# Kernel optimization log

Measured on AMD Instinct MI355X. Metric: run time of the kernel, lower is better.

## Reference

```python
import jax, jax.numpy as jnp
import numpy as np

# batched graph: B graphs, each with N_PER_G nodes, fixed in-degree DEG
N_NODES = 51200
N_PER_G = 100
B = 512
DEG = 16
E = N_NODES * DEG
D_IN = 100   # input node feature dim
H1 = 100     # gc1 out
D_G = 20     # gc2 out / graph embedding dim
D_K = 32
P2D = 200    # dim_self_feat
P3D = 100    # dim_3d_feat
D_OUT = 1
LN_EPS = 1e-5


def setup_inputs() -> dict:
    key = jax.random.key(0)
    ks = jax.random.split(key, 24)
    feat = jax.random.normal(ks[0], (N_NODES, D_IN), jnp.float32)
    # every node has exactly DEG in-edges; sources drawn within the same graph
    edge_dst = jnp.repeat(jnp.arange(N_NODES, dtype=jnp.int32), DEG)
    off = jax.random.randint(ks[1], (E,), 0, N_PER_G, jnp.int32)
    edge_src = (edge_dst // N_PER_G) * N_PER_G + off
    self_feat = jax.random.normal(ks[2], (B, P2D), jnp.float32)
    x3d = jax.random.normal(ks[3], (B, P3D), jnp.float32)

    def lin(k, o, i):
        return jax.random.normal(k, (o, i), jnp.float32) / np.sqrt(i).astype(np.float32)

    params = dict(
        W1=lin(ks[4], H1, D_IN), b1=jnp.zeros((H1,), jnp.float32),
        W2=lin(ks[5], D_G, H1), b2=jnp.zeros((D_G,), jnp.float32),
        Wq2=lin(ks[6], D_K, D_G), Wk2=lin(ks[7], D_K, P2D),
        Wv2=lin(ks[8], D_K, P2D), Wo2=lin(ks[9], D_G, D_K),
        g2=jnp.ones((D_G,), jnp.float32), be2=jnp.zeros((D_G,), jnp.float32),
        Wq3=lin(ks[10], D_K, D_G), Wk3=lin(ks[11], D_K, P3D),
        Wv3=lin(ks[12], D_K, P3D), Wo3=lin(ks[13], D_G, D_K),
        g3=jnp.ones((D_G,), jnp.float32), be3=jnp.zeros((D_G,), jnp.float32),
        Wf1=lin(ks[14], 10, D_G), bf1=jnp.zeros((10,), jnp.float32),
        Wf2=lin(ks[15], D_OUT, 10), bf2=jnp.zeros((D_OUT,), jnp.float32),
    )
    return dict(feat=feat, edge_src=edge_src, edge_dst=edge_dst,
                self_feat=self_feat, x3d=x3d, **params)


def _gcn(h, src, dst, W, b):
    # copy_u -> mailbox mean (every node has exactly DEG in-edges) -> Linear
    msg = h[src]                                              # [E, d] gather
    acc = jax.ops.segment_sum(msg, dst, num_segments=N_NODES) / DEG
    return acc @ W.T + b


def _cross_attn(hg, x, Wq, Wk, Wv, Wo, gamma, beta):
    # K,V are single tokens -> softmax over length-1 axis is identically 1
    # so Z = V @ Wo^T exactly (Q/Wq does not affect the output values).
    Z = (x @ Wv.T) @ Wo.T                                     # [B, d_g]
    y = hg + Z
    mu = jnp.mean(y, axis=-1, keepdims=True)
    var = jnp.mean((y - mu) ** 2, axis=-1, keepdims=True)
    hg_attn = (y - mu) / jnp.sqrt(var + LN_EPS) * gamma + beta
    A = jnp.ones((hg.shape[0], 1), y.dtype)                   # softmax of (B,1,1)
    return hg_attn, A


def reference(feat, edge_src, edge_dst, self_feat, x3d,
              W1, b1, W2, b2,
              Wq2, Wk2, Wv2, Wo2, g2, be2,
              Wq3, Wk3, Wv3, Wo3, g3, be3,
              Wf1, bf1, Wf2, bf2):
    h = jax.nn.relu(_gcn(feat, edge_src, edge_dst, W1, b1))   # [N, 100]
    h = jax.nn.relu(_gcn(h, edge_src, edge_dst, W2, b2))      # [N, 20]
    hg = h.reshape(B, N_PER_G, D_G).mean(axis=1)              # dgl.mean_nodes
    hg1, _ = _cross_attn(hg, self_feat, Wq2, Wk2, Wv2, Wo2, g2, be2)
    hg2, _ = _cross_attn(hg1, x3d, Wq3, Wk3, Wv3, Wo3, g3, be3)
    out = jax.nn.relu(hg2 @ Wf1.T + bf1)
    out = out @ Wf2.T + bf2                                   # [B, 1]
    return out
```

## Files before the change

kernel.cpp:

```cpp
#include <hip/hip_runtime.h>
#include <hip/hip_bf16.h>

#define LN_EPS 1e-5f

typedef __attribute__((ext_vector_type(8))) short bf16x8;
typedef __attribute__((ext_vector_type(4))) float f32x4;

#define S 136
#define OFF_F  0
#define OFF_A  13600
#define OFF_S  28832
#define OFF_T2 33184
#define FLT    37536
#define ARENA_U 39360

#define FSF  0
#define FX3  200
#define FB1  300
#define FB2  400
#define FG2  420
#define FBE2 440
#define FG3  460
#define FBE3 480
#define FWF1 500
#define FBF1 700
#define FWF2 712
#define FBF2 724
#define FV2  728
#define FV3  760
#define FZ2  792
#define FZ3  812
#define FHGP 832

__device__ __forceinline__ unsigned short bf16rne(float x) {
    union { float f; unsigned u; } v; v.f = x;
    unsigned r = (v.u + 0x7FFFu + ((v.u >> 16) & 1u)) >> 16;
    return (unsigned short)r;
}

__device__ __forceinline__ unsigned pk2(float a, float b) {
    __hip_bfloat162 h = __float22bfloat162_rn(float2{a, b});
    unsigned r; __builtin_memcpy(&r, &h, 4); return r;
}

__device__ __forceinline__ void st4bf(unsigned short* p, const f32x4 v) {
    *(uint2*)p = make_uint2(pk2(v[0], v[1]), pk2(v[2], v[3]));
}

__device__ __forceinline__ bf16x8 pk8(const float4 a, const float4 b) {
    union { bf16x8 v; uint4 u; } r;
    r.u = make_uint4(pk2(a.x, a.y), pk2(a.z, a.w), pk2(b.x, b.y), pk2(b.z, b.w));
    return r.v;
}

template<int NT>
__device__ __forceinline__ void gemm_row(const unsigned short* __restrict__ ar,
    int Abase, int Bbase, int mrow, int lm, int lq, f32x4 (&acc)[NT])
{
    #pragma unroll
    for (int ks = 0; ks < 4; ++ks) {
        const int k = ks * 32 + lq * 8;
        bf16x8 a = *(const bf16x8*)&ar[Abase + (mrow * 16 + lm) * S + k];
        #pragma unroll
        for (int n = 0; n < NT; ++n) {
            bf16x8 b = *(const bf16x8*)&ar[Bbase + (n * 16 + lm) * S + k];
            acc[n] = __builtin_amdgcn_mfma_f32_16x16x32_bf16(a, b, acc[n], 0, 0, 0);
        }
    }
}

__global__ __launch_bounds__(512, 4) void fused_net_v6(
    const float* __restrict__ feat, const int* __restrict__ edge_src,
    const float* __restrict__ self_feat, const float* __restrict__ x3d,
    const float* __restrict__ W1, const float* __restrict__ b1,
    const float* __restrict__ W2, const float* __restrict__ b2,
    const float* __restrict__ Wv2, const float* __restrict__ Wo2,
    const float* __restrict__ g2, const float* __restrict__ be2,
    const float* __restrict__ Wv3, const float* __restrict__ Wo3,
    const float* __restrict__ g3, const float* __restrict__ be3,
    const float* __restrict__ Wf1, const float* __restrict__ bf1,
    const float* __restrict__ Wf2, const float* __restrict__ bf2,
    float* __restrict__ out)
{
    __shared__ __align__(16) unsigned short ar[ARENA_U];
    float* fl = (float*)&ar[FLT];

    const int g    = blockIdx.x;
    const int tid  = threadIdx.x;
    const int w    = tid >> 6;
    const int lane = tid & 63;
    const int lm   = lane & 15;
    const int lq   = lane >> 4;

    int arow = -1;
    if (w == 7) arow = lane;
    else if (w == 6 && lane < 36) arow = 64 + lane;
    int er[16];
    bf16x8 afrag[4];

    {
        if (w < 7) {
            int am = w * 16 + lm; if (am > 99) am = 99;
            const float* frow = feat + g * 10000 + am * 100;
            #pragma unroll
            for (int ks = 0; ks < 3; ++ks) {
                const int k = ks * 32 + lq * 8;
                const float4 a = *(const float4*)&frow[k];
                const float4 b = *(const float4*)&frow[k + 4];
                afrag[ks] = pk8(a, b);
            }
            if (lq == 0) {
                const float4 a = *(const float4*)&frow[96];
                afrag[3] = pk8(a, make_float4(0.f, 0.f, 0.f, 0.f));
            } else {
                union { bf16x8 v; uint4 u; } z; z.u = make_uint4(0u,0u,0u,0u);
                afrag[3] = z.v;
            }
        }

        if (tid < 50) *(float4*)&fl[FSF + tid * 4] = *(const float4*)&self_feat[g * 200 + tid * 4];
        else if (tid < 75)  *(float4*)&fl[FX3 + (tid - 50) * 4] = *(const float4*)&x3d[g * 100 + (tid - 50) * 4];
        else if (tid < 100) *(float4*)&fl[FB1 + (tid - 75) * 4] = *(const float4*)&b1[(tid - 75) * 4];
        else if (tid < 105) *(float4*)&fl[FB2 + (tid - 100) * 4] = *(const float4*)&b2[(tid - 100) * 4];
        else if (tid < 110) *(float4*)&fl[FG2 + (tid - 105) * 4] = *(const float4*)&g2[(tid - 105) * 4];
        else if (tid < 115) *(float4*)&fl[FBE2 + (tid - 110) * 4] = *(const float4*)&be2[(tid - 110) * 4];
        else if (tid < 120) *(float4*)&fl[FG3 + (tid - 115) * 4] = *(const float4*)&g3[(tid - 115) * 4];
        else if (tid < 125) *(float4*)&fl[FBE3 + (tid - 120) * 4] = *(const float4*)&be3[(tid - 120) * 4];
        else if (tid < 175) *(float4*)&fl[FWF1 + (tid - 125) * 4] = *(const float4*)&Wf1[(tid - 125) * 4];
        else if (tid < 185) { const int j = tid - 175; fl[FBF1 + j] = bf1[j]; fl[FWF2 + j] = Wf2[j]; }
        else if (tid == 185) fl[FBF2] = bf2[0];
        if (tid >= 256 && tid < 336) fl[FHGP + (tid - 256)] = 0.f;

        if (arow >= 0) {
            const int* ep = edge_src + g * 1600 + arow * 16;
            int4 e;
            e = *(const int4*)&ep[0];  er[0]=e.x;  er[1]=e.y;  er[2]=e.z;  er[3]=e.w;
            e = *(const int4*)&ep[4];  er[4]=e.x;  er[5]=e.y;  er[6]=e.z;  er[7]=e.w;
            e = *(const int4*)&ep[8];  er[8]=e.x;  er[9]=e.y;  er[10]=e.z; er[11]=e.w;
            e = *(const int4*)&ep[12]; er[12]=e.x; er[13]=e.y; er[14]=e.z; er[15]=e.w;
            const int base = g * 100;
            #pragma unroll
            for (int i = 0; i < 16; ++i) er[i] -= base;
        }

        for (int i = tid; i < 2500; i += 512) {
            const int n = i / 25, k4 = (i % 25) * 4;
            const float4 v = *(const float4*)&W1[n * 100 + k4];
            *(uint2*)&ar[OFF_A + n * S + k4] = make_uint2(pk2(v.x, v.y), pk2(v.z, v.w));
        }
        for (int i = tid; i < 700; i += 512) {
            const int n = i / 7, j = (i % 7) * 4;
            *(uint2*)&ar[OFF_A + n * S + 100 + j] = make_uint2(0u, 0u);
        }
        for (int i = tid; i < 700; i += 512) {
            const int n = i / 7, j = (i % 7) * 4;
            *(uint2*)&ar[OFF_F + n * S + 100 + j] = make_uint2(0u, 0u);
        }
        for (int i = tid; i < 500; i += 512) {
            const int n = i / 25, k4 = (i % 25) * 4;
            const float4 v = *(const float4*)&W2[n * 100 + k4];
            *(uint2*)&ar[OFF_S + n * S + k4] = make_uint2(pk2(v.x, v.y), pk2(v.z, v.w));
        }
        for (int i = tid; i < 140; i += 512) {
            const int n = i / 7, j = (i % 7) * 4;
            *(uint2*)&ar[OFF_S + n * S + 100 + j] = make_uint2(0u, 0u);
        }
        for (int i = tid; i < 140; i += 512) {
            const int n = i / 7, j = (i % 7) * 4;
            *(uint2*)&ar[OFF_T2 + n * S + 100 + j] = make_uint2(0u, 0u);
        }
    }
    __syncthreads();

    f32x4 acc[7];
    {
        const f32x4 z = {0.f, 0.f, 0.f, 0.f};
        #pragma unroll
        for (int n = 0; n < 7; ++n) acc[n] = z;
    }
    if (w < 7) {
        #pragma unroll
        for (int ks = 0; ks < 4; ++ks) {
            const int k = ks * 32 + lq * 8;
            #pragma unroll
            for (int n = 0; n < 7; ++n) {
                bf16x8 b = *(const bf16x8*)&ar[OFF_A + (n * 16 + lm) * S + k];
                acc[n] = __builtin_amdgcn_mfma_f32_16x16x32_bf16(afrag[ks], b, acc[n], 0, 0, 0);
            }
        }
    } else {
        const int j = lane >> 1, h = lane & 1;
        {
            const float* wr = Wv2 + j * 200 + h * 100;
            float s = 0.f;
            for (int c = 0; c < 25; ++c) {
                const float4 a = *(const float4*)&wr[c * 4];
                const float4 x = *(const float4*)&fl[FSF + h * 100 + c * 4];
                s += a.x * x.x + a.y * x.y + a.z * x.z + a.w * x.w;
            }
            s += __shfl_xor(s, 1);
            if (h == 0) fl[FV2 + j] = s;
        }
        {
            const float* wr = Wv3 + j * 100;
            const int c0 = h ? 13 : 0, c1 = h ? 25 : 13;
            float s = 0.f;
            for (int c = c0; c < c1; ++c) {
                const float4 a = *(const float4*)&wr[c * 4];
                const float4 x = *(const float4*)&fl[FX3 + c * 4];
                s += a.x * x.x + a.y * x.y + a.z * x.z + a.w * x.w;
            }
            s += __shfl_xor(s, 1);
            if (h == 0) fl[FV3 + j] = s;
        }
    }
    __syncthreads();

    if (w < 7) {
        const int m0 = w * 16 + lq * 4;
        #pragma unroll
        for (int n = 0; n < 7; ++n) {
            const int cc = n * 16 + lm;
            if (cc < 100 && m0 <= 96) st4bf(&ar[OFF_F + cc * S + m0], acc[n]);
        }
    }
    if (arow >= 0) {
        const uint4 z4i = make_uint4(0u, 0u, 0u, 0u);
        const int st = arow & 7;
        #pragma unroll
        for (int pp = 0; pp < 17; ++pp) {
            int p = pp + st; if (p >= 17) p -= 17;
            *(uint4*)&ar[OFF_A + arow * S + p * 8] = z4i;
        }
        #pragma unroll
        for (int i = 0; i < 16; ++i) {
            int cnt = 0;
            #pragma unroll
            for (int j = 0; j < 16; ++j) cnt += (er[j] == er[i]);
            ar[OFF_A + arow * S + er[i]] = bf16rne((float)cnt * 0.0625f);
        }
    }
    __syncthreads();

    {
        const f32x4 z = {0.f, 0.f, 0.f, 0.f};
        #pragma unroll
        for (int n = 0; n < 7; ++n) acc[n] = z;
    }
    if (w < 7) {
        gemm_row<7>(ar, OFF_F, OFF_A, w, lm, lq, acc);
    } else {
        if (lane < 20) {
            const float* wr = Wo2 + lane * 32;
            float s = 0.f;
            #pragma unroll
            for (int c = 0; c < 8; ++c) {
                const float4 a = *(const float4*)&wr[c * 4];
                s += a.x * fl[FV2 + c * 4] + a.y * fl[FV2 + c * 4 + 1]
                   + a.z * fl[FV2 + c * 4 + 2] + a.w * fl[FV2 + c * 4 + 3];
            }
            fl[FZ2 + lane] = s;
        } else if (lane < 40) {
            const int j = lane - 20;
            const float* wr = Wo3 + j * 32;
            float s = 0.f;
            #pragma unroll
            for (int c = 0; c < 8; ++c) {
                const float4 a = *(const float4*)&wr[c * 4];
                s += a.x * fl[FV3 + c * 4] + a.y * fl[FV3 + c * 4 + 1]
                   + a.z * fl[FV3 + c * 4 + 2] + a.w * fl[FV3 + c * 4 + 3];
            }
            fl[FZ3 + j] = s;
        }
    }
    __syncthreads();

    if (w < 7) {
        const int m0 = w * 16 + lq * 4;
        if (m0 <= 96) {
            const float4 bb = *(const float4*)&fl[FB1 + m0];
            #pragma unroll
            for (int n = 0; n < 7; ++n) {
                const int cc = n * 16 + lm;
                if (cc < 100) {
                    f32x4 v = acc[n];
                    v[0] = fmaxf(v[0] + bb.x, 0.f); v[1] = fmaxf(v[1] + bb.y, 0.f);
                    v[2] = fmaxf(v[2] + bb.z, 0.f); v[3] = fmaxf(v[3] + bb.w, 0.f);
                    st4bf(&ar[OFF_F + cc * S + m0], v);
                }
            }
        }
    }
    __syncthreads();

    const int mt  = w & 1;
    const int ntA = w >> 1;
    const bool hasB = (w < 6);
    const int ntB = 4 + (w >> 1);
    {
        const f32x4 z = {0.f, 0.f, 0.f, 0.f};
        f32x4 cA = z, cB = z;
        #pragma unroll
        for (int ks = 0; ks < 4; ++ks) {
            const int k = ks * 32 + lq * 8;
            bf16x8 a = *(const bf16x8*)&ar[OFF_S + (mt * 16 + lm) * S + k];
            bf16x8 bA = *(const bf16x8*)&ar[OFF_F + (ntA * 16 + lm) * S + k];
            cA = __builtin_amdgcn_mfma_f32_16x16x32_bf16(a, bA, cA, 0, 0, 0);
            if (hasB) {
                bf16x8 bB = *(const bf16x8*)&ar[OFF_F + (ntB * 16 + lm) * S + k];
                cB = __builtin_amdgcn_mfma_f32_16x16x32_bf16(a, bB, cB, 0, 0, 0);
            }
        }
        const int ccA = ntA * 16 + lm;
        if (ccA < 100) {
            #pragma unroll
            for (int r = 0; r < 4; ++r) {
                const int f2 = mt * 16 + lq * 4 + r;
                if (f2 < 20) ar[OFF_T2 + f2 * S + ccA] = bf16rne(cA[r]);
            }
        }
        if (hasB) {
            const int ccB = ntB * 16 + lm;
            if (ccB < 100) {
                #pragma unroll
                for (int r = 0; r < 4; ++r) {
                    const int f2 = mt * 16 + lq * 4 + r;
                    if (f2 < 20) ar[OFF_T2 + f2 * S + ccB] = bf16rne(cB[r]);
                }
            }
        }
    }
    __syncthreads();

    {
        const f32x4 z = {0.f, 0.f, 0.f, 0.f};
        f32x4 cA = z, cB = z;
        #pragma unroll
        for (int ks = 0; ks < 4; ++ks) {
            const int k = ks * 32 + lq * 8;
            bf16x8 a = *(const bf16x8*)&ar[OFF_T2 + (mt * 16 + lm) * S + k];
            bf16x8 bA = *(const bf16x8*)&ar[OFF_A + (ntA * 16 + lm) * S + k];
            cA = __builtin_amdgcn_mfma_f32_16x16x32_bf16(a, bA, cA, 0, 0, 0);
            if (hasB) {
                bf16x8 bB = *(const bf16x8*)&ar[OFF_A + (ntB * 16 + lm) * S + k];
                cB = __builtin_amdgcn_mfma_f32_16x16x32_bf16(a, bB, cB, 0, 0, 0);
            }
        }
        const int ccA = ntA * 16 + lm;
        const int ccB = ntB * 16 + lm;
        #pragma unroll
        for (int r = 0; r < 4; ++r) {
            const int f2 = mt * 16 + lq * 4 + r;
            const bool fv = (f2 < 20);
            const float bias = fv ? fl[FB2 + (fv ? f2 : 0)] : 0.f;
            float val = (fv && ccA < 100) ? fmaxf(cA[r] + bias, 0.f) : 0.f;
            if (hasB && fv && ccB < 100) val += fmaxf(cB[r] + bias, 0.f);
            val += __shfl_xor(val, 1);
            val += __shfl_xor(val, 2);
            val += __shfl_xor(val, 4);
            val += __shfl_xor(val, 8);
            if (lm == 0 && fv) fl[FHGP + (w >> 1) * 20 + f2] = val;
        }
    }
    __syncthreads();

    if (tid < 64) {
        const int j = tid;
        float y = 0.f;
        if (j < 20) {
            y = fl[FHGP + j] + fl[FHGP + 20 + j] + fl[FHGP + 40 + j] + fl[FHGP + 60 + j];
            y = y * 0.01f + fl[FZ2 + j];
        }
        float s = y;
        s += __shfl_xor(s, 1); s += __shfl_xor(s, 2); s += __shfl_xor(s, 4);
        s += __shfl_xor(s, 8); s += __shfl_xor(s, 16);
        const float mu = s * 0.05f;
        float d = (j < 20) ? (y - mu) : 0.f;
        float v = d * d;
        v += __shfl_xor(v, 1); v += __shfl_xor(v, 2); v += __shfl_xor(v, 4);
        v += __shfl_xor(v, 8); v += __shfl_xor(v, 16);
        const float inv1 = 1.f / sqrtf(v * 0.05f + LN_EPS);
        float y2 = 0.f;
        if (j < 20) y2 = d * inv1 * fl[FG2 + j] + fl[FBE2 + j] + fl[FZ3 + j];
        float s2 = y2;
        s2 += __shfl_xor(s2, 1); s2 += __shfl_xor(s2, 2); s2 += __shfl_xor(s2, 4);
        s2 += __shfl_xor(s2, 8); s2 += __shfl_xor(s2, 16);
        const float mu2 = s2 * 0.05f;
        float d2 = (j < 20) ? (y2 - mu2) : 0.f;
        float v2 = d2 * d2;
        v2 += __shfl_xor(v2, 1); v2 += __shfl_xor(v2, 2); v2 += __shfl_xor(v2, 4);
        v2 += __shfl_xor(v2, 8); v2 += __shfl_xor(v2, 16);
        const float inv2 = 1.f / sqrtf(v2 * 0.05f + LN_EPS);
        float y3 = 0.f;
        if (j < 20) y3 = d2 * inv2 * fl[FG3 + j] + fl[FBE3 + j];

        float acc7 = 0.f;
        {
            const int js = (j < 10) ? j : 0;
            #pragma unroll
            for (int k = 0; k < 20; ++k) {
                const float yk = __shfl(y3, k);
                acc7 += fl[FWF1 + js * 20 + k] * yk;
            }
            const float bias = fl[FBF1 + js];
            const float w2v  = fl[FWF2 + js];
            acc7 = (j < 10) ? fmaxf(acc7 + bias, 0.f) * w2v : 0.f;
        }
        acc7 += __shfl_xor(acc7, 1); acc7 += __shfl_xor(acc7, 2);
        acc7 += __shfl_xor(acc7, 4); acc7 += __shfl_xor(acc7, 8);
        if (j == 0) out[g] = acc7 + fl[FBF2];
    }
}

extern "C" void kernel_launch(void* const* d_in, const int* in_sizes, int n_in,
                              void* d_out, int out_size, void* d_ws, size_t ws_size,
                              hipStream_t stream) {
    const float* feat      = (const float*)d_in[0];
    const int*   edge_src  = (const int*)  d_in[1];
    const float* self_feat = (const float*)d_in[3];
    const float* x3d       = (const float*)d_in[4];
    const float* W1  = (const float*)d_in[5];
    const float* b1  = (const float*)d_in[6];
    const float* W2  = (const float*)d_in[7];
    const float* b2  = (const float*)d_in[8];
    const float* Wv2 = (const float*)d_in[11];
    const float* Wo2 = (const float*)d_in[12];
    const float* g2  = (const float*)d_in[13];
    const float* be2 = (const float*)d_in[14];
    const float* Wv3 = (const float*)d_in[17];
    const float* Wo3 = (const float*)d_in[18];
    const float* g3  = (const float*)d_in[19];
    const float* be3 = (const float*)d_in[20];
    const float* Wf1 = (const float*)d_in[21];
    const float* bf1 = (const float*)d_in[22];
    const float* Wf2 = (const float*)d_in[23];
    const float* bf2 = (const float*)d_in[24];

    fused_net_v6<<<512, 512, 0, stream>>>(feat, edge_src, self_feat, x3d,
                                          W1, b1, W2, b2,
                                          Wv2, Wo2, g2, be2,
                                          Wv3, Wo3, g3, be3,
                                          Wf1, bf1, Wf2, bf2,
                                          (float*)d_out);
}
```

Baseline: 130.2 us.

## Load W1 fragments directly from global and merge prologue phases to drop barriers

The first GEMM now builds its B fragments for W1 directly from global memory into registers instead of staging W1 as bf16 in shared memory. That removes a barrier and lets the X@W1 product and the adjacency-matrix build run in the same phase. The cross-attention V projections read self_feat and x3d straight from global, and the adjacency rows are built by wave 7 with per-lane register edge lists. Two __syncthreads are removed, at the cost of redundant global W1 loads per wave, which the cache should serve.

```diff
diff --git a/kernel.cpp b/kernel.cpp
--- a/kernel.cpp
+++ b/kernel.cpp
@@ -14,8 +14,6 @@
 #define FLT    37536
 #define ARENA_U 39360
 
-#define FSF  0
-#define FX3  200
 #define FB1  300
 #define FB2  400
 #define FG2  420
@@ -69,7 +67,7 @@
     }
 }
 
-__global__ __launch_bounds__(512, 4) void fused_net_v6(
+__global__ __launch_bounds__(512, 4) void fused_net_v7(
     const float* __restrict__ feat, const int* __restrict__ edge_src,
     const float* __restrict__ self_feat, const float* __restrict__ x3d,
     const float* __restrict__ W1, const float* __restrict__ b1,
@@ -92,110 +90,121 @@
     const int lm   = lane & 15;
     const int lq   = lane >> 4;
 
-    int arow = -1;
-    if (w == 7) arow = lane;
-    else if (w == 6 && lane < 36) arow = 64 + lane;
-    int er[16];
-    bf16x8 afrag[4];
-
-    {
-        if (w < 7) {
+    if (tid < 25)       *(float4*)&fl[FB1 + tid * 4]          = *(const float4*)&b1[tid * 4];
+    else if (tid < 30)  *(float4*)&fl[FB2 + (tid - 25) * 4]   = *(const float4*)&b2[(tid - 25) * 4];
+    else if (tid < 35)  *(float4*)&fl[FG2 + (tid - 30) * 4]   = *(const float4*)&g2[(tid - 30) * 4];
+    else if (tid < 40)  *(float4*)&fl[FBE2 + (tid - 35) * 4]  = *(const float4*)&be2[(tid - 35) * 4];
+    else if (tid < 45)  *(float4*)&fl[FG3 + (tid - 40) * 4]   = *(const float4*)&g3[(tid - 40) * 4];
+    else if (tid < 50)  *(float4*)&fl[FBE3 + (tid - 45) * 4]  = *(const float4*)&be3[(tid - 45) * 4];
+    else if (tid < 100) *(float4*)&fl[FWF1 + (tid - 50) * 4]  = *(const float4*)&Wf1[(tid - 50) * 4];
+    else if (tid < 110) { const int j = tid - 100; fl[FBF1 + j] = bf1[j]; fl[FWF2 + j] = Wf2[j]; }
+    else if (tid == 110) fl[FBF2] = bf2[0];
+
+    if (w < 7) {
+        bf16x8 afrag[4];
+        {
             int am = w * 16 + lm; if (am > 99) am = 99;
             const float* frow = feat + g * 10000 + am * 100;
             #pragma unroll
             for (int ks = 0; ks < 3; ++ks) {
                 const int k = ks * 32 + lq * 8;
-                const float4 a = *(const float4*)&frow[k];
-                const float4 b = *(const float4*)&frow[k + 4];
-                afrag[ks] = pk8(a, b);
-            }
-            if (lq == 0) {
-                const float4 a = *(const float4*)&frow[96];
-                afrag[3] = pk8(a, make_float4(0.f, 0.f, 0.f, 0.f));
-            } else {
-                union { bf16x8 v; uint4 u; } z; z.u = make_uint4(0u,0u,0u,0u);
-                afrag[3] = z.v;
-            }
-        }
-
-        if (tid < 50) *(float4*)&fl[FSF + tid * 4] = *(const float4*)&self_feat[g * 200 + tid * 4];
-        else if (tid < 75)  *(float4*)&fl[FX3 + (tid - 50) * 4] = *(const float4*)&x3d[g * 100 + (tid - 50) * 4];
-        else if (tid < 100) *(float4*)&fl[FB1 + (tid - 75) * 4] = *(const float4*)&b1[(tid - 75) * 4];
-        else if (tid < 105) *(float4*)&fl[FB2 + (tid - 100) * 4] = *(const float4*)&b2[(tid - 100) * 4];
-        else if (tid < 110) *(float4*)&fl[FG2 + (tid - 105) * 4] = *(const float4*)&g2[(tid - 105) * 4];
-        else if (tid < 115) *(float4*)&fl[FBE2 + (tid - 110) * 4] = *(const float4*)&be2[(tid - 110) * 4];
-        else if (tid < 120) *(float4*)&fl[FG3 + (tid - 115) * 4] = *(const float4*)&g3[(tid - 115) * 4];
-        else if (tid < 125) *(float4*)&fl[FBE3 + (tid - 120) * 4] = *(const float4*)&be3[(tid - 120) * 4];
-        else if (tid < 175) *(float4*)&fl[FWF1 + (tid - 125) * 4] = *(const float4*)&Wf1[(tid - 125) * 4];
-        else if (tid < 185) { const int j = tid - 175; fl[FBF1 + j] = bf1[j]; fl[FWF2 + j] = Wf2[j]; }
-        else if (tid == 185) fl[FBF2] = bf2[0];
-        if (tid >= 256 && tid < 336) fl[FHGP + (tid - 256)] = 0.f;
-
-        if (arow >= 0) {
-            const int* ep = edge_src + g * 1600 + arow * 16;
-            int4 e;
-            e = *(const int4*)&ep[0];  er[0]=e.x;  er[1]=e.y;  er[2]=e.z;  er[3]=e.w;
-            e = *(const int4*)&ep[4];  er[4]=e.x;  er[5]=e.y;  er[6]=e.z;  er[7]=e.w;
-            e = *(const int4*)&ep[8];  er[8]=e.x;  er[9]=e.y;  er[10]=e.z; er[11]=e.w;
-            e = *(const int4*)&ep[12]; er[12]=e.x; er[13]=e.y; er[14]=e.z; er[15]=e.w;
-            const int base = g * 100;
-            #pragma unroll
-            for (int i = 0; i < 16; ++i) er[i] -= base;
-        }
-
-        for (int i = tid; i < 2500; i += 512) {
-            const int n = i / 25, k4 = (i % 25) * 4;
-            const float4 v = *(const float4*)&W1[n * 100 + k4];
-            *(uint2*)&ar[OFF_A + n * S + k4] = make_uint2(pk2(v.x, v.y), pk2(v.z, v.w));
-        }
-        for (int i = tid; i < 700; i += 512) {
-            const int n = i / 7, j = (i % 7) * 4;
-            *(uint2*)&ar[OFF_A + n * S + 100 + j] = make_uint2(0u, 0u);
-        }
-        for (int i = tid; i < 700; i += 512) {
-            const int n = i / 7, j = (i % 7) * 4;
-            *(uint2*)&ar[OFF_F + n * S + 100 + j] = make_uint2(0u, 0u);
-        }
-        for (int i = tid; i < 500; i += 512) {
+                afrag[ks] = pk8(*(const float4*)&frow[k], *(const float4*)&frow[k + 4]);
+            }
+            const float4 z4 = make_float4(0.f, 0.f, 0.f, 0.f);
+            afrag[3] = (lq == 0) ? pk8(*(const float4*)&frow[96], z4) : pk8(z4, z4);
+        }
+
+        for (int i = tid; i < 500; i += 448) {
             const int n = i / 25, k4 = (i % 25) * 4;
             const float4 v = *(const float4*)&W2[n * 100 + k4];
             *(uint2*)&ar[OFF_S + n * S + k4] = make_uint2(pk2(v.x, v.y), pk2(v.z, v.w));
         }
-        for (int i = tid; i < 140; i += 512) {
+        for (int i = tid; i < 140; i += 448) {
             const int n = i / 7, j = (i % 7) * 4;
             *(uint2*)&ar[OFF_S + n * S + 100 + j] = make_uint2(0u, 0u);
         }
-        for (int i = tid; i < 140; i += 512) {
+        for (int i = tid; i < 700; i += 448) {
+            const int n = i / 7, j = (i % 7) * 4;
+            *(uint2*)&ar[OFF_F + n * S + 100 + j] = make_uint2(0u, 0u);
+        }
+        for (int i = tid; i < 140; i += 448) {
             const int n = i / 7, j = (i % 7) * 4;
             *(uint2*)&ar[OFF_T2 + n * S + 100 + j] = make_uint2(0u, 0u);
         }
-    }
-    __syncthreads();
-
-    f32x4 acc[7];
-    {
-        const f32x4 z = {0.f, 0.f, 0.f, 0.f};
-        #pragma unroll
-        for (int n = 0; n < 7; ++n) acc[n] = z;
-    }
-    if (w < 7) {
-        #pragma unroll
-        for (int ks = 0; ks < 4; ++ks) {
+
+        f32x4 acc[7];
+        {
+            const f32x4 z = {0.f, 0.f, 0.f, 0.f};
+            #pragma unroll
+            for (int n = 0; n < 7; ++n) acc[n] = z;
+        }
+        #pragma unroll
+        for (int ks = 0; ks < 3; ++ks) {
             const int k = ks * 32 + lq * 8;
+            bf16x8 bf[7];
             #pragma unroll
             for (int n = 0; n < 7; ++n) {
-                bf16x8 b = *(const bf16x8*)&ar[OFF_A + (n * 16 + lm) * S + k];
-                acc[n] = __builtin_amdgcn_mfma_f32_16x16x32_bf16(afrag[ks], b, acc[n], 0, 0, 0);
+                int brow = n * 16 + lm; if (brow > 99) brow = 99;
+                const float* p = W1 + brow * 100 + k;
+                bf[n] = pk8(*(const float4*)p, *(const float4*)(p + 4));
+            }
+            #pragma unroll
+            for (int n = 0; n < 7; ++n)
+                acc[n] = __builtin_amdgcn_mfma_f32_16x16x32_bf16(afrag[ks], bf[n], acc[n], 0, 0, 0);
+        }
+        {
+            const float4 z4 = make_float4(0.f, 0.f, 0.f, 0.f);
+            bf16x8 bf[7];
+            #pragma unroll
+            for (int n = 0; n < 7; ++n) {
+                int brow = n * 16 + lm; if (brow > 99) brow = 99;
+                const float4 a = (lq == 0) ? *(const float4*)&W1[brow * 100 + 96] : z4;
+                bf[n] = pk8(a, z4);
+            }
+            #pragma unroll
+            for (int n = 0; n < 7; ++n)
+                acc[n] = __builtin_amdgcn_mfma_f32_16x16x32_bf16(afrag[3], bf[n], acc[n], 0, 0, 0);
+        }
+        {
+            const int m0 = w * 16 + lq * 4;
+            #pragma unroll
+            for (int n = 0; n < 7; ++n) {
+                const int cc = n * 16 + lm;
+                if (cc < 100 && m0 <= 96) st4bf(&ar[OFF_F + cc * S + m0], acc[n]);
             }
         }
     } else {
+        const int base = g * 100;
+        int e1[16], e2[16];
+        {
+            const int* ep = edge_src + g * 1600 + lane * 16;
+            int4 e;
+            e = *(const int4*)&ep[0];  e1[0]=e.x;  e1[1]=e.y;  e1[2]=e.z;  e1[3]=e.w;
+            e = *(const int4*)&ep[4];  e1[4]=e.x;  e1[5]=e.y;  e1[6]=e.z;  e1[7]=e.w;
+            e = *(const int4*)&ep[8];  e1[8]=e.x;  e1[9]=e.y;  e1[10]=e.z; e1[11]=e.w;
+            e = *(const int4*)&ep[12]; e1[12]=e.x; e1[13]=e.y; e1[14]=e.z; e1[15]=e.w;
+            #pragma unroll
+            for (int i = 0; i < 16; ++i) e1[i] -= base;
+        }
+        const bool r2 = (lane < 36);
+        if (r2) {
+            const int* ep = edge_src + g * 1600 + (64 + lane) * 16;
+            int4 e;
+            e = *(const int4*)&ep[0];  e2[0]=e.x;  e2[1]=e.y;  e2[2]=e.z;  e2[3]=e.w;
+            e = *(const int4*)&ep[4];  e2[4]=e.x;  e2[5]=e.y;  e2[6]=e.z;  e2[7]=e.w;
+            e = *(const int4*)&ep[8];  e2[8]=e.x;  e2[9]=e.y;  e2[10]=e.z; e2[11]=e.w;
+            e = *(const int4*)&ep[12]; e2[12]=e.x; e2[13]=e.y; e2[14]=e.z; e2[15]=e.w;
+            #pragma unroll
+            for (int i = 0; i < 16; ++i) e2[i] -= base;
+        }
         const int j = lane >> 1, h = lane & 1;
         {
             const float* wr = Wv2 + j * 200 + h * 100;
+            const float* xr = self_feat + g * 200 + h * 100;
             float s = 0.f;
             for (int c = 0; c < 25; ++c) {
                 const float4 a = *(const float4*)&wr[c * 4];
-                const float4 x = *(const float4*)&fl[FSF + h * 100 + c * 4];
+                const float4 x = *(const float4*)&xr[c * 4];
                 s += a.x * x.x + a.y * x.y + a.z * x.z + a.w * x.w;
             }
             s += __shfl_xor(s, 1);
@@ -203,53 +212,51 @@
         }
         {
             const float* wr = Wv3 + j * 100;
+            const float* xr = x3d + g * 100;
             const int c0 = h ? 13 : 0, c1 = h ? 25 : 13;
             float s = 0.f;
             for (int c = c0; c < c1; ++c) {
                 const float4 a = *(const float4*)&wr[c * 4];
-                const float4 x = *(const float4*)&fl[FX3 + c * 4];
+                const float4 x = *(const float4*)&xr[c * 4];
                 s += a.x * x.x + a.y * x.y + a.z * x.z + a.w * x.w;
             }
             s += __shfl_xor(s, 1);
             if (h == 0) fl[FV3 + j] = s;
         }
-    }
-    __syncthreads();
-
-    if (w < 7) {
-        const int m0 = w * 16 + lq * 4;
-        #pragma unroll
-        for (int n = 0; n < 7; ++n) {
-            const int cc = n * 16 + lm;
-            if (cc < 100 && m0 <= 96) st4bf(&ar[OFF_F + cc * S + m0], acc[n]);
-        }
-    }
-    if (arow >= 0) {
-        const uint4 z4i = make_uint4(0u, 0u, 0u, 0u);
-        const int st = arow & 7;
-        #pragma unroll
-        for (int pp = 0; pp < 17; ++pp) {
-            int p = pp + st; if (p >= 17) p -= 17;
-            *(uint4*)&ar[OFF_A + arow * S + p * 8] = z4i;
-        }
-        #pragma unroll
-        for (int i = 0; i < 16; ++i) {
-            int cnt = 0;
-            #pragma unroll
-            for (int j = 0; j < 16; ++j) cnt += (er[j] == er[i]);
-            ar[OFF_A + arow * S + er[i]] = bf16rne((float)cnt * 0.0625f);
-        }
-    }
-    __syncthreads();
-
-    {
-        const f32x4 z = {0.f, 0.f, 0.f, 0.f};
-        #pragma unroll
-        for (int n = 0; n < 7; ++n) acc[n] = z;
-    }
-    if (w < 7) {
-        gemm_row<7>(ar, OFF_F, OFF_A, w, lm, lq, acc);
-    } else {
+        {
+            const uint4 z4i = make_uint4(0u, 0u, 0u, 0u);
+            const int r = lane;
+            const int st = (r >> 3) % 17;
+            #pragma unroll
+            for (int pp = 0; pp < 17; ++pp) {
+                int p = pp + st; if (p >= 17) p -= 17;
+                *(uint4*)&ar[OFF_A + r * S + p * 8] = z4i;
+            }
+            #pragma unroll
+            for (int i = 0; i < 16; ++i) {
+                int cnt = 0;
+                #pragma unroll
+                for (int jj = 0; jj < 16; ++jj) cnt += (e1[jj] == e1[i]);
+                ar[OFF_A + r * S + e1[i]] = bf16rne((float)cnt * 0.0625f);
+            }
+        }
+        if (r2) {
+            const uint4 z4i = make_uint4(0u, 0u, 0u, 0u);
+            const int r = 64 + lane;
+            const int st = (r >> 3) % 17;
+            #pragma unroll
+            for (int pp = 0; pp < 17; ++pp) {
+                int p = pp + st; if (p >= 17) p -= 17;
+                *(uint4*)&ar[OFF_A + r * S + p * 8] = z4i;
+            }
+            #pragma unroll
+            for (int i = 0; i < 16; ++i) {
+                int cnt = 0;
+                #pragma unroll
+                for (int jj = 0; jj < 16; ++jj) cnt += (e2[jj] == e2[i]);
+                ar[OFF_A + r * S + e2[i]] = bf16rne((float)cnt * 0.0625f);
+            }
+        }
         if (lane < 20) {
             const float* wr = Wo2 + lane * 32;
             float s = 0.f;
@@ -261,8 +268,8 @@
             }
             fl[FZ2 + lane] = s;
         } else if (lane < 40) {
-            const int j = lane - 20;
-            const float* wr = Wo3 + j * 32;
+            const int jz = lane - 20;
+            const float* wr = Wo3 + jz * 32;
             float s = 0.f;
             #pragma unroll
             for (int c = 0; c < 8; ++c) {
@@ -270,9 +277,18 @@
                 s += a.x * fl[FV3 + c * 4] + a.y * fl[FV3 + c * 4 + 1]
                    + a.z * fl[FV3 + c * 4 + 2] + a.w * fl[FV3 + c * 4 + 3];
             }
-            fl[FZ3 + j] = s;
-        }
-    }
+            fl[FZ3 + jz] = s;
+        }
+    }
+    __syncthreads();
+
+    f32x4 acc2[7];
+    {
+        const f32x4 z = {0.f, 0.f, 0.f, 0.f};
+        #pragma unroll
+        for (int n = 0; n < 7; ++n) acc2[n] = z;
+    }
+    if (w < 7) gemm_row<7>(ar, OFF_F, OFF_A, w, lm, lq, acc2);
     __syncthreads();
 
     if (w < 7) {
@@ -283,7 +299,7 @@
             for (int n = 0; n < 7; ++n) {
                 const int cc = n * 16 + lm;
                 if (cc < 100) {
-                    f32x4 v = acc[n];
+                    f32x4 v = acc2[n];
                     v[0] = fmaxf(v[0] + bb.x, 0.f); v[1] = fmaxf(v[1] + bb.y, 0.f);
                     v[2] = fmaxf(v[2] + bb.z, 0.f); v[3] = fmaxf(v[3] + bb.w, 0.f);
                     st4bf(&ar[OFF_F + cc * S + m0], v);
@@ -436,7 +452,7 @@
     const float* Wf2 = (const float*)d_in[23];
     const float* bf2 = (const float*)d_in[24];
 
-    fused_net_v6<<<512, 512, 0, stream>>>(feat, edge_src, self_feat, x3d,
+    fused_net_v7<<<512, 512, 0, stream>>>(feat, edge_src, self_feat, x3d,
                                           W1, b1, W2, b2,
                                           Wv2, Wo2, g2, be2,
                                           Wv3, Wo3, g3, be3,
```

Measured after the change: 136.9 us. +5.2%, slower.
